# Kernel optimization log

Measured on AMD Instinct MI355X. Metric: run time of the kernel, lower is better.

The kernel has to match this reference:

```python
import jax, jax.numpy as jnp
import numpy as np

IN_FEATURES = 4096
OUT_FEATURES = 4096
NUM_FRAGMENTS = 32
FRAGMENT_SIZE = IN_FEATURES // NUM_FRAGMENTS  # 128
COMPRESSED = 512
BATCH = 8192


def setup_inputs() -> dict:
    key = jax.random.key(0)
    k_x, k_sel, k_exp, k_c1, k_c2 = jax.random.split(key, 5)
    inv_sqrt_fs = 1.0 / np.sqrt(FRAGMENT_SIZE)
    return {
        "x": jax.random.normal(k_x, (BATCH, IN_FEATURES), dtype=jnp.float32),
        "selector_weights": jax.random.normal(k_sel, (NUM_FRAGMENTS, FRAGMENT_SIZE), dtype=jnp.float32) * inv_sqrt_fs,
        "expert_weights": jax.random.normal(k_exp, (NUM_FRAGMENTS, FRAGMENT_SIZE, OUT_FEATURES), dtype=jnp.float32) * inv_sqrt_fs,
        # store Linear weights as [in, out] so forward is x @ W
        "w_compressor": jax.random.normal(k_c1, (IN_FEATURES, COMPRESSED), dtype=jnp.float32) * (1.0 / np.sqrt(IN_FEATURES)),
        "w_compressed": jax.random.normal(k_c2, (COMPRESSED, OUT_FEATURES), dtype=jnp.float32) * (1.0 / np.sqrt(COMPRESSED)),
    }


def reference(x, selector_weights, expert_weights, w_compressor, w_compressed):
    B, D = x.shape
    F, S = selector_weights.shape  # num_fragments, fragment_size
    x_frag = x.reshape(B, F, S)
    # selector scores and soft routing probs over fragments
    scores = jnp.einsum('bfi,fi->bf', x_frag, selector_weights)
    probs = jax.nn.softmax(scores, axis=1)  # [B, F]
    # soft-routed expert output: weight fragments by probs first to avoid a [B,F,O] intermediate
    x_weighted = x_frag * probs[:, :, None]  # [B, F, S]
    expert_out = jnp.einsum('bfi,fio->bo', x_weighted, expert_weights)  # [B, O]
    # fragment mask mapped to full feature dim: mask = 1 - probs[fragment_mapping]
    mask = 1.0 - jnp.repeat(probs, S, axis=1)  # [B, D]
    masked_input = x * mask
    compressed_out = (masked_input @ w_compressor) @ w_compressed  # [B, O]
    return expert_out + compressed_out
```

## Files before the change

### kernel.cpp

```cpp
#include <hip/hip_runtime.h>
#include <hip/hip_bf16.h>
#include <stdint.h>

#define BATCH 8192
#define IN_F  4096
#define OUT_F 4096
#define NFRAG 32
#define FSIZE 128
#define COMP  512

typedef float f32x4 __attribute__((ext_vector_type(4)));
typedef short bf16x8 __attribute__((ext_vector_type(8)));

__device__ __forceinline__ unsigned short f2bf(float f) {
  union { float f; unsigned u; } v; v.f = f;
  return (unsigned short)((v.u + 0x7FFFu + ((v.u >> 16) & 1u)) >> 16);
}
__device__ __forceinline__ unsigned pack2(float a, float b) {
  return (unsigned)f2bf(a) | ((unsigned)f2bf(b) << 16);
}

typedef const __attribute__((address_space(1))) unsigned* as1_u32p;
typedef __attribute__((address_space(3))) unsigned* as3_u32p;

__device__ __forceinline__ void lds_load16(const void* g, void* l) {
  __builtin_amdgcn_global_load_lds((as1_u32p)(uintptr_t)g, (as3_u32p)(uintptr_t)l, 16, 0, 0);
}

__global__ __launch_bounds__(256) void k_route(
    const float* __restrict__ x, const float* __restrict__ sel,
    unsigned short* __restrict__ xw, unsigned short* __restrict__ xm) {
  __shared__ float red[256];
  __shared__ float sc[NFRAG];
  const int b = blockIdx.x;
  const int t = threadIdx.x;
  const float* xr = x + (size_t)b * IN_F;
  const int frag = t >> 3;

  float4 v0 = *(const float4*)&xr[t * 16 + 0];
  float4 v1 = *(const float4*)&xr[t * 16 + 4];
  float4 v2 = *(const float4*)&xr[t * 16 + 8];
  float4 v3 = *(const float4*)&xr[t * 16 + 12];
  const float* sw = sel + frag * FSIZE + (t & 7) * 16;
  float4 s0 = *(const float4*)&sw[0];
  float4 s1 = *(const float4*)&sw[4];
  float4 s2 = *(const float4*)&sw[8];
  float4 s3 = *(const float4*)&sw[12];
  float d = v0.x*s0.x + v0.y*s0.y + v0.z*s0.z + v0.w*s0.w
          + v1.x*s1.x + v1.y*s1.y + v1.z*s1.z + v1.w*s1.w
          + v2.x*s2.x + v2.y*s2.y + v2.z*s2.z + v2.w*s2.w
          + v3.x*s3.x + v3.y*s3.y + v3.z*s3.z + v3.w*s3.w;
  red[t] = d;
  __syncthreads();
  if (t < NFRAG) {
    float s = 0.f;
#pragma unroll
    for (int j = 0; j < 8; ++j) s += red[t * 8 + j];
    sc[t] = s;
  }
  __syncthreads();
  float mx = sc[0];
#pragma unroll
  for (int f = 1; f < NFRAG; ++f) mx = fmaxf(mx, sc[f]);
  float den = 0.f;
#pragma unroll
  for (int f = 0; f < NFRAG; ++f) den += __expf(sc[f] - mx);
  const float p = __expf(sc[frag] - mx) / den;
  const float q = 1.f - p;

  const size_t base = (size_t)b * IN_F + (size_t)t * 16;
  uint4 w;
  w.x = pack2(v0.x*p, v0.y*p); w.y = pack2(v0.z*p, v0.w*p);
  w.z = pack2(v1.x*p, v1.y*p); w.w = pack2(v1.z*p, v1.w*p);
  *(uint4*)&xw[base] = w;
  w.x = pack2(v2.x*p, v2.y*p); w.y = pack2(v2.z*p, v2.w*p);
  w.z = pack2(v3.x*p, v3.y*p); w.w = pack2(v3.z*p, v3.w*p);
  *(uint4*)&xw[base + 8] = w;
  w.x = pack2(v0.x*q, v0.y*q); w.y = pack2(v0.z*q, v0.w*q);
  w.z = pack2(v1.x*q, v1.y*q); w.w = pack2(v1.z*q, v1.w*q);
  *(uint4*)&xm[base] = w;
  w.x = pack2(v2.x*q, v2.y*q); w.y = pack2(v2.z*q, v2.w*q);
  w.z = pack2(v3.x*q, v3.y*q); w.w = pack2(v3.z*q, v3.w*q);
  *(uint4*)&xm[base + 8] = w;
}

__global__ __launch_bounds__(256) void k_transpose_bf16(
    const float* __restrict__ src, unsigned short* __restrict__ dst, int R, int C) {
  __shared__ float tile[64][65];
  const int t = threadIdx.x;
  const int c0 = blockIdx.x * 64, r0 = blockIdx.y * 64;
#pragma unroll
  for (int i = 0; i < 4; ++i) {
    const int q = i * 256 + t;
    const int row = q >> 4;
    const int col = (q & 15) << 2;
    float4 v = *(const float4*)&src[(size_t)(r0 + row) * C + c0 + col];
    tile[row][col + 0] = v.x; tile[row][col + 1] = v.y;
    tile[row][col + 2] = v.z; tile[row][col + 3] = v.w;
  }
  __syncthreads();
#pragma unroll
  for (int i = 0; i < 4; ++i) {
    const int q = i * 256 + t;
    const int orow = q >> 4;
    const int oc = (q & 15) << 2;
    ushort4 o;
    o.x = f2bf(tile[oc + 0][orow]);
    o.y = f2bf(tile[oc + 1][orow]);
    o.z = f2bf(tile[oc + 2][orow]);
    o.w = f2bf(tile[oc + 3][orow]);
    *(ushort4*)&dst[(size_t)(c0 + orow) * R + r0 + oc] = o;
  }
}

#define BM 128
#define BN 128
#define BK 64

template <int EPI>
__global__ __launch_bounds__(256) void k_gemm_bt(
    const unsigned short* __restrict__ A, const unsigned short* __restrict__ Bt,
    void* __restrict__ Cp, int M, int N, int K) {
  __shared__ unsigned short lA[BM * BK];
  __shared__ unsigned short lB[BN * BK];
  const int t = threadIdx.x;
  const int lane = t & 63;
  const int wave = t >> 6;
  const int wr = wave >> 1, wc = wave & 1;
  const int hi = lane >> 4, lo = lane & 15;
  const int bm = blockIdx.y * BM, bn = blockIdx.x * BN;

  f32x4 acc[4][4] = {};

  for (int kt = 0; kt < K; kt += BK) {
#pragma unroll
    for (int i = 0; i < 4; ++i) {
      const int c = i * 256 + t;
      const int row = c >> 3, cc = c & 7;
      lds_load16(&A [(size_t)(bm + row) * K + kt + cc * 8], (char*)lA + c * 16);
      lds_load16(&Bt[(size_t)(bn + row) * K + kt + cc * 8], (char*)lB + c * 16);
    }
    __syncthreads();
#pragma unroll
    for (int kk = 0; kk < BK; kk += 32) {
      bf16x8 af[4], bfr[4];
#pragma unroll
      for (int m = 0; m < 4; ++m)
        af[m] = *(const bf16x8*)&lA[(wr * 64 + m * 16 + lo) * BK + kk + hi * 8];
#pragma unroll
      for (int n = 0; n < 4; ++n)
        bfr[n] = *(const bf16x8*)&lB[(wc * 64 + n * 16 + lo) * BK + kk + hi * 8];
#pragma unroll
      for (int m = 0; m < 4; ++m)
#pragma unroll
        for (int n = 0; n < 4; ++n)
          acc[m][n] = __builtin_amdgcn_mfma_f32_16x16x32_bf16(af[m], bfr[n], acc[m][n], 0, 0, 0);
    }
    __syncthreads();
  }

  float* Cf = (float*)Cp;
  unsigned short* Cb = (unsigned short*)Cp;
#pragma unroll
  for (int m = 0; m < 4; ++m)
#pragma unroll
    for (int n = 0; n < 4; ++n)
#pragma unroll
      for (int r = 0; r < 4; ++r) {
        const int row = bm + wr * 64 + m * 16 + hi * 4 + r;
        const int col = bn + wc * 64 + n * 16 + lo;
        const size_t idx = (size_t)row * N + col;
        if constexpr (EPI == 0)      Cf[idx] = acc[m][n][r];
        else if constexpr (EPI == 1) Cf[idx] += acc[m][n][r];
        else                         Cb[idx] = f2bf(acc[m][n][r]);
      }
}

#define G_SLOT  16384
#define G_STRIDE 32768
#define G_LDS   98304

template <int EPI>
__global__ __launch_bounds__(512, 2) void k_gemm256(
    const unsigned short* __restrict__ A, const unsigned short* __restrict__ Bt,
    float* __restrict__ C, int M, int N, int K) {
  extern __shared__ char lds[];
  const int t = threadIdx.x;
  const int lane = t & 63;
  const int wid = t >> 6;
  const int wr = wid >> 2;
  const int wc = wid & 3;
  const int lo = lane & 15, hi = lane >> 4;

  const int nwg = gridDim.x;
  const int chunk = nwg >> 3;
  const int remap = ((int)blockIdx.x & 7) * chunk + ((int)blockIdx.x >> 3);
  const int nx = N >> 8;
  const int bm = (remap / nx) << 8;
  const int bn = (remap % nx) << 8;

  const int NT = K >> 5;

  const int c0 = t,       r0 = c0 >> 2, s0 = (c0 & 3) ^ ((r0 >> 1) & 3);
  const int c1 = t + 512, r1 = c1 >> 2, s1 = (c1 & 3) ^ ((r1 >> 1) & 3);
  const unsigned short* Ap0 = A  + (size_t)(bm + r0) * K + s0 * 8;
  const unsigned short* Ap1 = A  + (size_t)(bm + r1) * K + s1 * 8;
  const unsigned short* Bp0 = Bt + (size_t)(bn + r0) * K + s0 * 8;
  const unsigned short* Bp1 = Bt + (size_t)(bn + r1) * K + s1 * 8;

  const int ksl = ((hi ^ ((lo >> 1) & 3)) << 4);
  const int aBase = wr * 8192 + lo * 64 + ksl;
  const int bBase = G_SLOT + wc * 4096 + lo * 64 + ksl;

  f32x4 acc[8][4] = {};

#define STAGE(tt_) do {                                            \
    char* _b = lds + ((tt_) % 3) * G_STRIDE;                       \
    const int _kt = (tt_) << 5;                                    \
    lds_load16(Ap0 + _kt, _b + c0 * 16);                           \
    lds_load16(Ap1 + _kt, _b + c1 * 16);                           \
    lds_load16(Bp0 + _kt, _b + G_SLOT + c0 * 16);                  \
    lds_load16(Bp1 + _kt, _b + G_SLOT + c1 * 16);                  \
  } while (0)

  STAGE(0);
  STAGE(1);
  asm volatile("s_waitcnt vmcnt(4)" ::: "memory");
  __builtin_amdgcn_sched_barrier(0);
  __builtin_amdgcn_s_barrier();
  __builtin_amdgcn_sched_barrier(0);

  for (int tt = 0; tt < NT; ++tt) {
    if (tt + 2 < NT) STAGE(tt + 2);
    const char* sa = lds + (tt % 3) * G_STRIDE;
    bf16x8 a[8], b[4];
#pragma unroll
    for (int n = 0; n < 4; ++n) b[n] = *(const bf16x8*)(sa + bBase + n * 1024);
#pragma unroll
    for (int m = 0; m < 8; ++m) a[m] = *(const bf16x8*)(sa + aBase + m * 1024);
    asm volatile("s_waitcnt lgkmcnt(0)" ::: "memory");
    __builtin_amdgcn_sched_barrier(0);
    __builtin_amdgcn_s_setprio(1);
#pragma unroll
    for (int m = 0; m < 8; ++m)
#pragma unroll
      for (int n = 0; n < 4; ++n)
        acc[m][n] = __builtin_amdgcn_mfma_f32_16x16x32_bf16(a[m], b[n], acc[m][n], 0, 0, 0);
    __builtin_amdgcn_s_setprio(0);
    if (tt + 1 < NT) {
      if (tt + 2 < NT) { asm volatile("s_waitcnt vmcnt(4)" ::: "memory"); }
      else             { asm volatile("s_waitcnt vmcnt(0)" ::: "memory"); }
      __builtin_amdgcn_sched_barrier(0);
      __builtin_amdgcn_s_barrier();
      __builtin_amdgcn_sched_barrier(0);
    }
  }
#undef STAGE

#pragma unroll
  for (int m = 0; m < 8; ++m)
#pragma unroll
    for (int n = 0; n < 4; ++n)
#pragma unroll
      for (int r = 0; r < 4; ++r) {
        const int row = bm + wr * 128 + m * 16 + hi * 4 + r;
        const int col = bn + wc * 64 + n * 16 + lo;
        const size_t idx = (size_t)row * N + col;
        if constexpr (EPI == 0) C[idx] = acc[m][n][r];
        else                    C[idx] += acc[m][n][r];
      }
}

extern "C" void kernel_launch(void* const* d_in, const int* in_sizes, int n_in,
                              void* d_out, int out_size, void* d_ws, size_t ws_size,
                              hipStream_t stream) {
  const float* x   = (const float*)d_in[0];
  const float* sel = (const float*)d_in[1];
  const float* ew  = (const float*)d_in[2];
  const float* wc1 = (const float*)d_in[3];
  const float* wc2 = (const float*)d_in[4];
  float* out = (float*)d_out;

  char* ws = (char*)d_ws;
  unsigned short* xw   = (unsigned short*)(ws);
  unsigned short* xm   = (unsigned short*)(ws + 67108864);
  unsigned short* w1t  = xm;
  unsigned short* tbuf = (unsigned short*)(ws + 134217728);
  unsigned short* w1ct = (unsigned short*)(ws + 142606336);
  unsigned short* w2ct = (unsigned short*)(ws + 146800640);

  (void)hipFuncSetAttribute((const void*)k_gemm256<0>,
                            hipFuncAttributeMaxDynamicSharedMemorySize, G_LDS);
  (void)hipFuncSetAttribute((const void*)k_gemm256<1>,
                            hipFuncAttributeMaxDynamicSharedMemorySize, G_LDS);

  k_route<<<BATCH, 256, 0, stream>>>(x, sel, xw, xm);
  k_transpose_bf16<<<dim3(COMP  / 64, IN_F / 64), 256, 0, stream>>>(wc1, w1ct, IN_F, COMP);
  k_transpose_bf16<<<dim3(OUT_F / 64, COMP / 64), 256, 0, stream>>>(wc2, w2ct, COMP, OUT_F);
  k_gemm_bt<2><<<dim3(COMP / BN, BATCH / BM), 256, 0, stream>>>(xm, w1ct, (void*)tbuf, BATCH, COMP, IN_F);
  k_transpose_bf16<<<dim3(OUT_F / 64, IN_F / 64), 256, 0, stream>>>(ew, w1t, IN_F, OUT_F);
  k_gemm256<0><<<(BATCH / 256) * (OUT_F / 256), 512, G_LDS, stream>>>(xw, w1t, out, BATCH, OUT_F, IN_F);
  k_gemm256<1><<<(BATCH / 256) * (OUT_F / 256), 512, G_LDS, stream>>>(tbuf, w2ct, out, BATCH, OUT_F, COMP);
}
```

Measured before the change: 751.9 us.

## Concatenate expert and compressed GEMMs along K into one GEMM

The routing kernel now writes the prob-weighted activations into a [B, 4608] concatenated buffer, and the first compressor GEMM writes its bf16 output into the last 512 columns of the same buffer. The expert and second-compressor weights are transposed side by side into one [4096, 4608] matrix. A single GEMM with K=4608 then replaces two GEMMs and skips the separate read-modify-write of the fp32 output. The GEMM main loop also drops its explicit lgkmcnt wait and sched barrier and raises priority earlier, leaving LDS wait placement to the compiler. The xm and btcat workspace regions overlap, which is safe only because xm is fully consumed before btcat is written.

```diff
diff --git a/kernel.cpp b/kernel.cpp
--- a/kernel.cpp
+++ b/kernel.cpp
@@ -8,6 +8,7 @@
 #define NFRAG 32
 #define FSIZE 128
 #define COMP  512
+#define KCAT  4608
 
 typedef float f32x4 __attribute__((ext_vector_type(4)));
 typedef short bf16x8 __attribute__((ext_vector_type(8)));
@@ -68,24 +69,26 @@
   const float p = __expf(sc[frag] - mx) / den;
   const float q = 1.f - p;
 
-  const size_t base = (size_t)b * IN_F + (size_t)t * 16;
+  const size_t bw = (size_t)b * KCAT + (size_t)t * 16;
+  const size_t bm_ = (size_t)b * IN_F + (size_t)t * 16;
   uint4 w;
   w.x = pack2(v0.x*p, v0.y*p); w.y = pack2(v0.z*p, v0.w*p);
   w.z = pack2(v1.x*p, v1.y*p); w.w = pack2(v1.z*p, v1.w*p);
-  *(uint4*)&xw[base] = w;
+  *(uint4*)&xw[bw] = w;
   w.x = pack2(v2.x*p, v2.y*p); w.y = pack2(v2.z*p, v2.w*p);
   w.z = pack2(v3.x*p, v3.y*p); w.w = pack2(v3.z*p, v3.w*p);
-  *(uint4*)&xw[base + 8] = w;
+  *(uint4*)&xw[bw + 8] = w;
   w.x = pack2(v0.x*q, v0.y*q); w.y = pack2(v0.z*q, v0.w*q);
   w.z = pack2(v1.x*q, v1.y*q); w.w = pack2(v1.z*q, v1.w*q);
-  *(uint4*)&xm[base] = w;
+  *(uint4*)&xm[bm_] = w;
   w.x = pack2(v2.x*q, v2.y*q); w.y = pack2(v2.z*q, v2.w*q);
   w.z = pack2(v3.x*q, v3.y*q); w.w = pack2(v3.z*q, v3.w*q);
-  *(uint4*)&xm[base + 8] = w;
+  *(uint4*)&xm[bm_ + 8] = w;
 }
 
 __global__ __launch_bounds__(256) void k_transpose_bf16(
-    const float* __restrict__ src, unsigned short* __restrict__ dst, int R, int C) {
+    const float* __restrict__ src, unsigned short* __restrict__ dst,
+    int R, int C, int ldd) {
   __shared__ float tile[64][65];
   const int t = threadIdx.x;
   const int c0 = blockIdx.x * 64, r0 = blockIdx.y * 64;
@@ -109,7 +112,7 @@
     o.y = f2bf(tile[oc + 1][orow]);
     o.z = f2bf(tile[oc + 2][orow]);
     o.w = f2bf(tile[oc + 3][orow]);
-    *(ushort4*)&dst[(size_t)(c0 + orow) * R + r0 + oc] = o;
+    *(ushort4*)&dst[(size_t)(c0 + orow) * ldd + r0 + oc] = o;
   }
 }
 
@@ -119,8 +122,9 @@
 
 template <int EPI>
 __global__ __launch_bounds__(256) void k_gemm_bt(
-    const unsigned short* __restrict__ A, const unsigned short* __restrict__ Bt,
-    void* __restrict__ Cp, int M, int N, int K) {
+    const unsigned short* __restrict__ A, int lda,
+    const unsigned short* __restrict__ Bt, int ldb,
+    void* __restrict__ Cp, int ldc, int M, int N, int K) {
   __shared__ unsigned short lA[BM * BK];
   __shared__ unsigned short lB[BN * BK];
   const int t = threadIdx.x;
@@ -137,8 +141,8 @@
     for (int i = 0; i < 4; ++i) {
       const int c = i * 256 + t;
       const int row = c >> 3, cc = c & 7;
-      lds_load16(&A [(size_t)(bm + row) * K + kt + cc * 8], (char*)lA + c * 16);
-      lds_load16(&Bt[(size_t)(bn + row) * K + kt + cc * 8], (char*)lB + c * 16);
+      lds_load16(&A [(size_t)(bm + row) * lda + kt + cc * 8], (char*)lA + c * 16);
+      lds_load16(&Bt[(size_t)(bn + row) * ldb + kt + cc * 8], (char*)lB + c * 16);
     }
     __syncthreads();
 #pragma unroll
@@ -169,7 +173,7 @@
       for (int r = 0; r < 4; ++r) {
         const int row = bm + wr * 64 + m * 16 + hi * 4 + r;
         const int col = bn + wc * 64 + n * 16 + lo;
-        const size_t idx = (size_t)row * N + col;
+        const size_t idx = (size_t)row * ldc + col;
         if constexpr (EPI == 0)      Cf[idx] = acc[m][n][r];
         else if constexpr (EPI == 1) Cf[idx] += acc[m][n][r];
         else                         Cb[idx] = f2bf(acc[m][n][r]);
@@ -180,9 +184,9 @@
 #define G_STRIDE 32768
 #define G_LDS   98304
 
-template <int EPI>
 __global__ __launch_bounds__(512, 2) void k_gemm256(
-    const unsigned short* __restrict__ A, const unsigned short* __restrict__ Bt,
+    const unsigned short* __restrict__ A, int lda,
+    const unsigned short* __restrict__ Bt, int ldb,
     float* __restrict__ C, int M, int N, int K) {
   extern __shared__ char lds[];
   const int t = threadIdx.x;
@@ -203,10 +207,10 @@
 
   const int c0 = t,       r0 = c0 >> 2, s0 = (c0 & 3) ^ ((r0 >> 1) & 3);
   const int c1 = t + 512, r1 = c1 >> 2, s1 = (c1 & 3) ^ ((r1 >> 1) & 3);
-  const unsigned short* Ap0 = A  + (size_t)(bm + r0) * K + s0 * 8;
-  const unsigned short* Ap1 = A  + (size_t)(bm + r1) * K + s1 * 8;
-  const unsigned short* Bp0 = Bt + (size_t)(bn + r0) * K + s0 * 8;
-  const unsigned short* Bp1 = Bt + (size_t)(bn + r1) * K + s1 * 8;
+  const unsigned short* Ap0 = A  + (size_t)(bm + r0) * lda + s0 * 8;
+  const unsigned short* Ap1 = A  + (size_t)(bm + r1) * lda + s1 * 8;
+  const unsigned short* Bp0 = Bt + (size_t)(bn + r0) * ldb + s0 * 8;
+  const unsigned short* Bp1 = Bt + (size_t)(bn + r1) * ldb + s1 * 8;
 
   const int ksl = ((hi ^ ((lo >> 1) & 3)) << 4);
   const int aBase = wr * 8192 + lo * 64 + ksl;
@@ -232,15 +236,13 @@
 
   for (int tt = 0; tt < NT; ++tt) {
     if (tt + 2 < NT) STAGE(tt + 2);
+    __builtin_amdgcn_s_setprio(1);
     const char* sa = lds + (tt % 3) * G_STRIDE;
     bf16x8 a[8], b[4];
 #pragma unroll
     for (int n = 0; n < 4; ++n) b[n] = *(const bf16x8*)(sa + bBase + n * 1024);
 #pragma unroll
     for (int m = 0; m < 8; ++m) a[m] = *(const bf16x8*)(sa + aBase + m * 1024);
-    asm volatile("s_waitcnt lgkmcnt(0)" ::: "memory");
-    __builtin_amdgcn_sched_barrier(0);
-    __builtin_amdgcn_s_setprio(1);
 #pragma unroll
     for (int m = 0; m < 8; ++m)
 #pragma unroll
@@ -265,9 +267,7 @@
       for (int r = 0; r < 4; ++r) {
         const int row = bm + wr * 128 + m * 16 + hi * 4 + r;
         const int col = bn + wc * 64 + n * 16 + lo;
-        const size_t idx = (size_t)row * N + col;
-        if constexpr (EPI == 0) C[idx] = acc[m][n][r];
-        else                    C[idx] += acc[m][n][r];
+        C[(size_t)row * N + col] = acc[m][n][r];
       }
 }
 
@@ -282,23 +282,20 @@
   float* out = (float*)d_out;
 
   char* ws = (char*)d_ws;
-  unsigned short* xw   = (unsigned short*)(ws);
-  unsigned short* xm   = (unsigned short*)(ws + 67108864);
-  unsigned short* w1t  = xm;
-  unsigned short* tbuf = (unsigned short*)(ws + 134217728);
-  unsigned short* w1ct = (unsigned short*)(ws + 142606336);
-  unsigned short* w2ct = (unsigned short*)(ws + 146800640);
-
-  (void)hipFuncSetAttribute((const void*)k_gemm256<0>,
+  unsigned short* xcat  = (unsigned short*)(ws);
+  unsigned short* xm    = (unsigned short*)(ws + 75497472);
+  unsigned short* btcat = (unsigned short*)(ws + 75497472);
+  unsigned short* w1ct  = (unsigned short*)(ws + 142606336);
+
+  (void)hipFuncSetAttribute((const void*)k_gemm256,
                             hipFuncAttributeMaxDynamicSharedMemorySize, G_LDS);
-  (void)hipFuncSetAttribute((const void*)k_gemm256<1>,
-                            hipFuncAttributeMaxDynamicSharedMemorySize, G_LDS);
-
-  k_route<<<BATCH, 256, 0, stream>>>(x, sel, xw, xm);
-  k_transpose_bf16<<<dim3(COMP  / 64, IN_F / 64), 256, 0, stream>>>(wc1, w1ct, IN_F, COMP);
-  k_transpose_bf16<<<dim3(OUT_F / 64, COMP / 64), 256, 0, stream>>>(wc2, w2ct, COMP, OUT_F);
-  k_gemm_bt<2><<<dim3(COMP / BN, BATCH / BM), 256, 0, stream>>>(xm, w1ct, (void*)tbuf, BATCH, COMP, IN_F);
-  k_transpose_bf16<<<dim3(OUT_F / 64, IN_F / 64), 256, 0, stream>>>(ew, w1t, IN_F, OUT_F);
-  k_gemm256<0><<<(BATCH / 256) * (OUT_F / 256), 512, G_LDS, stream>>>(xw, w1t, out, BATCH, OUT_F, IN_F);
-  k_gemm256<1><<<(BATCH / 256) * (OUT_F / 256), 512, G_LDS, stream>>>(tbuf, w2ct, out, BATCH, OUT_F, COMP);
-}
+
+  k_route<<<BATCH, 256, 0, stream>>>(x, sel, xcat, xm);
+  k_transpose_bf16<<<dim3(COMP / 64, IN_F / 64), 256, 0, stream>>>(wc1, w1ct, IN_F, COMP, IN_F);
+  k_gemm_bt<2><<<dim3(COMP / BN, BATCH / BM), 256, 0, stream>>>(
+      xm, IN_F, w1ct, IN_F, (void*)(xcat + IN_F), KCAT, BATCH, COMP, IN_F);
+  k_transpose_bf16<<<dim3(OUT_F / 64, IN_F / 64), 256, 0, stream>>>(ew, btcat, IN_F, OUT_F, KCAT);
+  k_transpose_bf16<<<dim3(OUT_F / 64, COMP / 64), 256, 0, stream>>>(wc2, btcat + IN_F, COMP, OUT_F, KCAT);
+  k_gemm256<<<(BATCH / 256) * (OUT_F / 256), 512, G_LDS, stream>>>(
+      xcat, KCAT, btcat, KCAT, out, BATCH, OUT_F, KCAT);
+}
```

Result: faster. 675.3 us (-10.2%).
